# Performance work log

Hardware: AMD Instinct MI355X
Metric: run time of the kernel (lower is better)

## Reference

```python
import jax, jax.numpy as jnp
import numpy as np
import math

HEADS = 32
GROUPS = 8
HEAD_DIM = 64
HIDDEN = 2048
B, S = 2, 2048


def _rope(x, freqs_cis):
    # x: (..., S, head_dim); freqs_cis: (S, head_dim) -> interleaved cos/sin pattern
    x_even = x[..., ::2]
    x_odd = x[..., 1::2]
    cos = freqs_cis[..., ::2]
    sin = freqs_cis[..., 1::2]
    r_even = x_even * cos - x_odd * sin
    r_odd = x_even * sin + x_odd * cos
    return jnp.stack([r_even, r_odd], axis=-1).reshape(x.shape)


def setup_inputs() -> dict:
    key = jax.random.key(0)
    ks = jax.random.split(key, 12)
    scale = 1.0 / math.sqrt(HIDDEN)
    x = jax.random.normal(ks[0], (B, S, HIDDEN), dtype=jnp.float32)
    freqs_cis = jax.random.uniform(ks[1], (S, HEAD_DIM), dtype=jnp.float32)
    causal = jnp.tril(jnp.ones((S, S), dtype=bool))
    mask = jnp.where(causal, 0.0, -1e9).astype(jnp.float32)
    kv_dims = HEAD_DIM * GROUPS
    wq = jax.random.normal(ks[2], (HIDDEN, HIDDEN), jnp.float32) * scale
    bq = jnp.zeros((HIDDEN,), jnp.float32)
    wk = jax.random.normal(ks[3], (kv_dims, HIDDEN), jnp.float32) * scale
    bk = jnp.zeros((kv_dims,), jnp.float32)
    wv = jax.random.normal(ks[4], (kv_dims, HIDDEN), jnp.float32) * scale
    bv = jnp.zeros((kv_dims,), jnp.float32)
    wo = jax.random.normal(ks[5], (HIDDEN, HIDDEN), jnp.float32) * scale
    bo = jnp.zeros((HIDDEN,), jnp.float32)
    return dict(x=x, freqs_cis=freqs_cis, mask=mask, wq=wq, bq=bq,
                wk=wk, bk=bk, wv=wv, bv=bv, wo=wo, bo=bo)


def reference(x, freqs_cis, mask, wq, bq, wk, bk, wv, bv, wo, bo):
    b, s, h = x.shape
    rep = HEADS // GROUPS
    q = x @ wq.T + bq                      # (B,S,H)
    k = x @ wk.T + bk                      # (B,S,G*hd)
    v = x @ wv.T + bv
    q = q.reshape(b, s, HEADS, HEAD_DIM).transpose(0, 2, 1, 3)   # (B,Hh,S,hd)
    k = k.reshape(b, s, GROUPS, HEAD_DIM).transpose(0, 2, 1, 3)  # (B,G,S,hd)
    v = v.reshape(b, s, GROUPS, HEAD_DIM).transpose(0, 2, 1, 3)
    q = _rope(q, freqs_cis)
    k = _rope(k, freqs_cis)
    # GQA: group q heads instead of materially repeating K/V
    qg = q.reshape(b, GROUPS, rep, s, HEAD_DIM)
    scores = jnp.einsum('bgrsd,bgtd->bgrst', qg, k) / math.sqrt(HEAD_DIM)
    scores = scores + mask                 # broadcast (S,S)
    attn = jax.nn.softmax(scores, axis=-1)
    out = jnp.einsum('bgrst,bgtd->bgrsd', attn, v)
    out = out.reshape(b, HEADS, s, HEAD_DIM).transpose(0, 2, 1, 3).reshape(b, s, h)
    return out @ wo.T + bo
```

## Files before the change

### kernel.cpp

```cpp
#include <hip/hip_runtime.h>

#define S_LEN 2048
#define HID   2048
#define NQH   32
#define NKV   8
#define HD    64

typedef __bf16 bf16x8 __attribute__((ext_vector_type(8)));
typedef __bf16 bf16x4 __attribute__((ext_vector_type(4)));
typedef float  f32x4  __attribute__((ext_vector_type(4)));

#define MFMA16(a, b, c) __builtin_amdgcn_mfma_f32_16x16x32_bf16(a, b, c, 0, 0, 0)

__device__ __forceinline__ void async_copy16(const void* g, void* l) {
  __builtin_amdgcn_global_load_lds(
      (const __attribute__((address_space(1))) unsigned int*)g,
      (__attribute__((address_space(3))) unsigned int*)l, 16, 0, 0);
}

__global__ void cast_all_k(const float* __restrict__ x,  const float* __restrict__ wq,
                           const float* __restrict__ wk, const float* __restrict__ wv,
                           const float* __restrict__ wo,
                           __bf16* __restrict__ xb,  __bf16* __restrict__ wqb,
                           __bf16* __restrict__ wkb, __bf16* __restrict__ wvb,
                           __bf16* __restrict__ wob) {
  int bid = blockIdx.x;
  const float* in; __bf16* out; int base;
  if (bid < 8192)       { in = x;  out = xb;  base = bid; }
  else if (bid < 12288) { in = wq; out = wqb; base = bid - 8192; }
  else if (bid < 13312) { in = wk; out = wkb; base = bid - 12288; }
  else if (bid < 14336) { in = wv; out = wvb; base = bid - 13312; }
  else                  { in = wo; out = wob; base = bid - 14336; }
  int i = (base * 256 + threadIdx.x) * 4;
  float4 v = *(const float4*)(in + i);
  bf16x4 o;
  o[0] = (__bf16)v.x; o[1] = (__bf16)v.y; o[2] = (__bf16)v.z; o[3] = (__bf16)v.w;
  *(bf16x4*)(out + i) = o;
}

__device__ __forceinline__ void gemm_core(const __bf16* __restrict__ A, const __bf16* __restrict__ B,
                                          int m0, int n0, int K,
                                          __bf16 (&Asm)[128][32], __bf16 (&Bsm)[128][32],
                                          f32x4 (&acc)[4][4]) {
  const int tid = threadIdx.x, wave = tid >> 6, lane = tid & 63;
  const int l15 = lane & 15, quad = lane >> 4;
  const int wr = wave >> 1, wc = wave & 1;
  const int lrow = lane >> 2, lcol = (lane & 3) * 8;

  const __bf16* ag = A + (size_t)(m0 + wave * 32 + lrow) * K + lcol;
  const __bf16* bg = B + (size_t)(n0 + wave * 32 + lrow) * K + lcol;
  __bf16* al = &Asm[wave * 32][0];
  __bf16* bl = &Bsm[wave * 32][0];
  const size_t rowstep = (size_t)16 * K;

  for (int kt = 0; kt < K; kt += 32) {
    __syncthreads();
    async_copy16(ag + kt, al);
    async_copy16(ag + kt + rowstep, al + 16 * 32);
    async_copy16(bg + kt, bl);
    async_copy16(bg + kt + rowstep, bl + 16 * 32);
    __syncthreads();
    bf16x8 af[4], bfr[4];
#pragma unroll
    for (int mt = 0; mt < 4; mt++)
      af[mt] = *(const bf16x8*)&Asm[wr * 64 + mt * 16 + l15][quad * 8];
#pragma unroll
    for (int nt = 0; nt < 4; nt++)
      bfr[nt] = *(const bf16x8*)&Bsm[wc * 64 + nt * 16 + l15][quad * 8];
#pragma unroll
    for (int mt = 0; mt < 4; mt++)
#pragma unroll
      for (int nt = 0; nt < 4; nt++)
        acc[mt][nt] = MFMA16(af[mt], bfr[nt], acc[mt][nt]);
  }
}

__global__ __launch_bounds__(256) void gemm_qkv_k(const __bf16* __restrict__ xb,
    const __bf16* __restrict__ wqb, const __bf16* __restrict__ wkb, const __bf16* __restrict__ wvb,
    const float* __restrict__ bq, const float* __restrict__ bk, const float* __restrict__ bv,
    const float* __restrict__ fr,
    __bf16* __restrict__ Qb, __bf16* __restrict__ Kb, __bf16* __restrict__ Vt) {
  __shared__ __align__(16) __bf16 Asm[128][32];
  __shared__ __align__(16) __bf16 Bsm[128][32];
  const int by = blockIdx.y;
  const int m0 = blockIdx.x * 128;
  const __bf16* B; const float* bias; int n0;
  int mode;
  if (by < 16)      { B = wqb; bias = bq; n0 = by * 128;        mode = 0; }
  else if (by < 20) { B = wkb; bias = bk; n0 = (by - 16) * 128; mode = 1; }
  else              { B = wvb; bias = bv; n0 = (by - 20) * 128; mode = 2; }

  f32x4 acc[4][4] = {};
  gemm_core(xb, B, m0, n0, HID, Asm, Bsm, acc);

  const int tid = threadIdx.x, wave = tid >> 6, lane = tid & 63;
  const int l15 = lane & 15, quad = lane >> 4;
  const int wr = wave >> 1, wc = wave & 1;

  if (mode == 2) {
#pragma unroll
    for (int nt = 0; nt < 4; nt++) {
      int col = n0 + wc * 64 + nt * 16 + l15;
      int g = col >> 6, d = col & 63;
      float bv2 = bias[col];
#pragma unroll
      for (int mt = 0; mt < 4; mt++) {
        int row = m0 + wr * 64 + mt * 16 + quad * 4;
        int b = row >> 11, s = row & 2047;
        bf16x4 o;
#pragma unroll
        for (int r = 0; r < 4; r++) o[r] = (__bf16)(acc[mt][nt][r] + bv2);
        *(bf16x4*)(Vt + (((size_t)(b * NKV + g) * HD + d)) * S_LEN + s) = o;
      }
    }
  } else {
    const float scale = (mode == 0) ? 0.125f * 1.44269504f : 1.0f;
    const int ldc = (mode == 0) ? HID : 512;
    __bf16* C = (mode == 0) ? Qb : Kb;
    const int dpar = l15 & 1;
#pragma unroll
    for (int nt = 0; nt < 4; nt++) {
      int col = n0 + wc * 64 + nt * 16 + l15;
      int d = col & 63;
      float bv2 = bias[col];
#pragma unroll
      for (int mt = 0; mt < 4; mt++) {
        int row = m0 + wr * 64 + mt * 16 + quad * 4;
        int s = row & 2047;
#pragma unroll
        for (int r = 0; r < 4; r++) {
          float v = acc[mt][nt][r] + bv2;
          float p = __shfl_xor(v, 1, 64);
          float f = fr[(size_t)(s + r) * HD + d];
          float fp = __shfl_xor(f, 1, 64);
          float o = dpar ? (p * f + v * fp) : (v * f - p * fp);
          C[(size_t)(row + r) * ldc + col] = (__bf16)(o * scale);
        }
      }
    }
  }
}

__global__ __launch_bounds__(256) void gemm_out_k(const __bf16* __restrict__ A,
    const __bf16* __restrict__ Bw, const float* __restrict__ bias, float* __restrict__ C) {
  __shared__ __align__(16) __bf16 Asm[128][32];
  __shared__ __align__(16) __bf16 Bsm[128][32];
  const int m0 = blockIdx.x * 128, n0 = blockIdx.y * 128;
  f32x4 acc[4][4] = {};
  gemm_core(A, Bw, m0, n0, HID, Asm, Bsm, acc);
  const int tid = threadIdx.x, wave = tid >> 6, lane = tid & 63;
  const int l15 = lane & 15, quad = lane >> 4;
  const int wr = wave >> 1, wc = wave & 1;
#pragma unroll
  for (int nt = 0; nt < 4; nt++) {
    int col = n0 + wc * 64 + nt * 16 + l15;
    float bv = bias[col];
#pragma unroll
    for (int mt = 0; mt < 4; mt++) {
      int row = m0 + wr * 64 + mt * 16 + quad * 4;
#pragma unroll
      for (int r = 0; r < 4; r++)
        C[(size_t)(row + r) * HID + col] = acc[mt][nt][r] + bv;
    }
  }
}

__global__ __launch_bounds__(256) void flash_k(const __bf16* __restrict__ Q,
                                               const __bf16* __restrict__ K,
                                               const __bf16* __restrict__ Vt,
                                               __bf16* __restrict__ O) {
  __shared__ __align__(16) __bf16 Ksm[64][64];
  __shared__ __align__(16) __bf16 Vsm[64][64];
  __shared__ __align__(16) __bf16 Psm[4][32][64];
  const int tid = threadIdx.x;
  const int wave = tid >> 6, lane = tid & 63;
  const int l15 = lane & 15, quad = lane >> 4;
  const int x7 = l15 & 7;
  const int bh = blockIdx.x;
  const int qt = 15 - blockIdx.y;
  const int b = bh >> 5, h = bh & 31, g = h >> 2;
  const int q0 = qt * 128;
  const int wq0 = q0 + wave * 32;

  bf16x8 qf[2][2];
#pragma unroll
  for (int mt = 0; mt < 2; mt++) {
    const __bf16* qp = Q + ((size_t)(b * S_LEN + wq0 + mt * 16 + l15)) * HID + h * HD + quad * 8;
    qf[mt][0] = *(const bf16x8*)qp;
    qf[mt][1] = *(const bf16x8*)(qp + 32);
  }

  f32x4 acc[2][4] = {};
  float rsum[2][4] = {};

  const int srow = tid >> 2, sc = (tid & 3) * 16;
  const int r7 = srow & 7;
  const int w0 = (((sc >> 3))     ^ r7) * 8;
  const int w1 = (((sc >> 3) + 1) ^ r7) * 8;

  const __bf16* kbase = K + ((size_t)b * S_LEN) * (NKV * HD) + g * HD;
  const __bf16* vrow  = Vt + (((size_t)b * NKV + g) * HD + srow) * S_LEN;

  const int tmax = 2 * qt + 1;
  uint4 k0, k1, v0, v1;
  {
    const __bf16* kp = kbase + (size_t)srow * (NKV * HD) + sc;
    k0 = *(const uint4*)kp; k1 = *(const uint4*)(kp + 8);
    const __bf16* vp = vrow + sc;
    v0 = *(const uint4*)vp; v1 = *(const uint4*)(vp + 8);
  }

  for (int t = 0; t <= tmax; t++) {
    const int kv0 = t * 64;
    __syncthreads();
    *(uint4*)&Ksm[srow][w0] = k0;
    *(uint4*)&Ksm[srow][w1] = k1;
    *(uint4*)&Vsm[srow][w0] = v0;
    *(uint4*)&Vsm[srow][w1] = v1;
    if (t < tmax) {
      const int kv0n = kv0 + 64;
      const __bf16* kp = kbase + (size_t)(kv0n + srow) * (NKV * HD) + sc;
      k0 = *(const uint4*)kp; k1 = *(const uint4*)(kp + 8);
      const __bf16* vp = vrow + kv0n + sc;
      v0 = *(const uint4*)vp; v1 = *(const uint4*)(vp + 8);
    }
    __syncthreads();

    if (kv0 > wq0 + 31) continue;

    bf16x8 kf[2][4];
#pragma unroll
    for (int ks = 0; ks < 2; ks++)
#pragma unroll
      for (int nt = 0; nt < 4; nt++)
        kf[ks][nt] = *(const bf16x8*)&Ksm[nt * 16 + l15][((ks * 4 + quad) ^ x7) * 8];

    const bool domask = (kv0 + 63 > wq0);
#pragma unroll
    for (int mt = 0; mt < 2; mt++) {
      f32x4 sacc[4] = {};
#pragma unroll
      for (int nt = 0; nt < 4; nt++) {
        sacc[nt] = MFMA16(qf[mt][0], kf[0][nt], sacc[nt]);
        sacc[nt] = MFMA16(qf[mt][1], kf[1][nt], sacc[nt]);
      }
#pragma unroll
      for (int nt = 0; nt < 4; nt++) {
        int kv = kv0 + nt * 16 + l15;
        int qr = wq0 + mt * 16 + quad * 4;
#pragma unroll
        for (int r = 0; r < 4; r++) {
          float p = __builtin_exp2f(sacc[nt][r]);
          if (domask && kv > qr + r) p = 0.f;
          rsum[mt][r] += p;
          int prow = mt * 16 + quad * 4 + r;
          Psm[wave][prow][(((nt * 2 + (l15 >> 3)) ^ (prow & 7)) * 8) + (l15 & 7)] = (__bf16)p;
        }
      }
    }

#pragma unroll
    for (int ks = 0; ks < 2; ks++) {
      bf16x8 vf[4];
#pragma unroll
      for (int nt = 0; nt < 4; nt++)
        vf[nt] = *(const bf16x8*)&Vsm[nt * 16 + l15][((ks * 4 + quad) ^ x7) * 8];
#pragma unroll
      for (int mt = 0; mt < 2; mt++) {
        bf16x8 pf = *(const bf16x8*)&Psm[wave][mt * 16 + l15][((ks * 4 + quad) ^ x7) * 8];
#pragma unroll
        for (int nt = 0; nt < 4; nt++)
          acc[mt][nt] = MFMA16(pf, vf[nt], acc[mt][nt]);
      }
    }
  }

#pragma unroll
  for (int mt = 0; mt < 2; mt++)
#pragma unroll
    for (int off = 1; off < 16; off <<= 1)
#pragma unroll
      for (int r = 0; r < 4; r++)
        rsum[mt][r] += __shfl_xor(rsum[mt][r], off, 64);

#pragma unroll
  for (int mt = 0; mt < 2; mt++) {
    __bf16* op = O + ((size_t)(b * S_LEN + wq0 + mt * 16 + quad * 4)) * HID + h * HD;
    float inv[4];
#pragma unroll
    for (int r = 0; r < 4; r++) inv[r] = 1.f / rsum[mt][r];
#pragma unroll
    for (int nt = 0; nt < 4; nt++)
#pragma unroll
      for (int r = 0; r < 4; r++)
        op[(size_t)r * HID + nt * 16 + l15] = (__bf16)(acc[mt][nt][r] * inv[r]);
  }
}

extern "C" void kernel_launch(void* const* d_in, const int* in_sizes, int n_in,
                              void* d_out, int out_size, void* d_ws, size_t ws_size,
                              hipStream_t stream) {
  (void)in_sizes; (void)n_in; (void)out_size; (void)ws_size;
  const float* x  = (const float*)d_in[0];
  const float* fr = (const float*)d_in[1];
  const float* wq = (const float*)d_in[3];
  const float* bq = (const float*)d_in[4];
  const float* wk = (const float*)d_in[5];
  const float* bk = (const float*)d_in[6];
  const float* wv = (const float*)d_in[7];
  const float* bv = (const float*)d_in[8];
  const float* wo = (const float*)d_in[9];
  const float* bo = (const float*)d_in[10];
  float* out = (float*)d_out;
  char* ws = (char*)d_ws;

  __bf16* xb  = (__bf16*)(ws);
  __bf16* wqb = (__bf16*)(ws + ((size_t)16 << 20));
  __bf16* wkb = (__bf16*)(ws + ((size_t)24 << 20));
  __bf16* wvb = (__bf16*)(ws + ((size_t)26 << 20));
  __bf16* wob = (__bf16*)(ws + ((size_t)28 << 20));
  __bf16* Qb  = (__bf16*)(ws + ((size_t)36 << 20));
  __bf16* Kb  = (__bf16*)(ws + ((size_t)52 << 20));
  __bf16* Vtb = (__bf16*)(ws + ((size_t)60 << 20));
  __bf16* Ab  = (__bf16*)(ws + ((size_t)64 << 20));

  cast_all_k<<<18432, 256, 0, stream>>>(x, wq, wk, wv, wo, xb, wqb, wkb, wvb, wob);

  gemm_qkv_k<<<dim3(32, 24), 256, 0, stream>>>(xb, wqb, wkb, wvb, bq, bk, bv, fr, Qb, Kb, Vtb);

  flash_k<<<dim3(64, 16), 256, 0, stream>>>(Qb, Kb, Vtb, Ab);

  gemm_out_k<<<dim3(32, 16), 256, 0, stream>>>(Ab, wob, bo, out);
}
```

Before: 358.8 us.

## Compute softmax row sums with MFMA against ones and precompute LDS byte offsets

The per-element float row-sum accumulation and the final cross-lane shuffle reduction are replaced by an extra MFMA that multiplies the bf16 P tile by a vector of ones. The row sums therefore come from the same rounded P values that feed P@V. LDS addressing for K, V and P moves to precomputed byte offsets, and the global K/V pointers are advanced incrementally, which trims address arithmetic in the inner loop. The cost is one extra MFMA per P fragment, and the normalizer now sums bf16-rounded probabilities, a small numerical change.

```diff
diff --git a/kernel.cpp b/kernel.cpp
--- a/kernel.cpp
+++ b/kernel.cpp
@@ -169,18 +169,17 @@
                                                const __bf16* __restrict__ K,
                                                const __bf16* __restrict__ Vt,
                                                __bf16* __restrict__ O) {
-  __shared__ __align__(16) __bf16 Ksm[64][64];
-  __shared__ __align__(16) __bf16 Vsm[64][64];
-  __shared__ __align__(16) __bf16 Psm[4][32][64];
+  __shared__ __align__(64) __bf16 Ksm[64][64];
+  __shared__ __align__(64) __bf16 Vsm[64][64];
+  __shared__ __align__(64) __bf16 Psm[4][32][64];
   const int tid = threadIdx.x;
   const int wave = tid >> 6, lane = tid & 63;
   const int l15 = lane & 15, quad = lane >> 4;
-  const int x7 = l15 & 7;
+  const int x7 = l15 & 7, l15h = l15 >> 3;
   const int bh = blockIdx.x;
   const int qt = 15 - blockIdx.y;
   const int b = bh >> 5, h = bh & 31, g = h >> 2;
-  const int q0 = qt * 128;
-  const int wq0 = q0 + wave * 32;
+  const int wq0 = qt * 128 + wave * 32;
 
   bf16x8 qf[2][2];
 #pragma unroll
@@ -189,27 +188,37 @@
     qf[mt][0] = *(const bf16x8*)qp;
     qf[mt][1] = *(const bf16x8*)(qp + 32);
   }
+  bf16x8 ones;
+#pragma unroll
+  for (int j = 0; j < 8; j++) ones[j] = (__bf16)1.0f;
 
   f32x4 acc[2][4] = {};
-  float rsum[2][4] = {};
+  f32x4 accs[2] = {};
 
   const int srow = tid >> 2, sc = (tid & 3) * 16;
   const int r7 = srow & 7;
   const int w0 = (((sc >> 3))     ^ r7) * 8;
   const int w1 = (((sc >> 3) + 1) ^ r7) * 8;
 
-  const __bf16* kbase = K + ((size_t)b * S_LEN) * (NKV * HD) + g * HD;
-  const __bf16* vrow  = Vt + (((size_t)b * NKV + g) * HD + srow) * S_LEN;
+  char* kbp = (char*)&Ksm[0][0];
+  char* vbp = (char*)&Vsm[0][0];
+  char* pbp = (char*)&Psm[0][0][0];
+  int kr[2], pr[2], pw[4];
+#pragma unroll
+  for (int ks = 0; ks < 2; ks++) {
+    kr[ks] = l15 * 128 + (((ks * 4 + quad) ^ x7) * 16);
+    pr[ks] = wave * 4096 + kr[ks];
+  }
+#pragma unroll
+  for (int nt = 0; nt < 4; nt++)
+    pw[nt] = wave * 4096 + quad * 512 + x7 * 2 + (((2 * nt + l15h) ^ ((quad & 1) * 4)) * 16);
+
+  const __bf16* kp = K + ((size_t)b * S_LEN + srow) * (NKV * HD) + g * HD + sc;
+  const __bf16* vp = Vt + (((size_t)b * NKV + g) * HD + srow) * S_LEN + sc;
+  uint4 k0 = *(const uint4*)kp, k1 = *(const uint4*)(kp + 8);
+  uint4 v0 = *(const uint4*)vp, v1 = *(const uint4*)(vp + 8);
 
   const int tmax = 2 * qt + 1;
-  uint4 k0, k1, v0, v1;
-  {
-    const __bf16* kp = kbase + (size_t)srow * (NKV * HD) + sc;
-    k0 = *(const uint4*)kp; k1 = *(const uint4*)(kp + 8);
-    const __bf16* vp = vrow + sc;
-    v0 = *(const uint4*)vp; v1 = *(const uint4*)(vp + 8);
-  }
-
   for (int t = 0; t <= tmax; t++) {
     const int kv0 = t * 64;
     __syncthreads();
@@ -218,10 +227,8 @@
     *(uint4*)&Vsm[srow][w0] = v0;
     *(uint4*)&Vsm[srow][w1] = v1;
     if (t < tmax) {
-      const int kv0n = kv0 + 64;
-      const __bf16* kp = kbase + (size_t)(kv0n + srow) * (NKV * HD) + sc;
+      kp += 64 * NKV * HD;  vp += 64;
       k0 = *(const uint4*)kp; k1 = *(const uint4*)(kp + 8);
-      const __bf16* vp = vrow + kv0n + sc;
       v0 = *(const uint4*)vp; v1 = *(const uint4*)(vp + 8);
     }
     __syncthreads();
@@ -233,7 +240,7 @@
     for (int ks = 0; ks < 2; ks++)
 #pragma unroll
       for (int nt = 0; nt < 4; nt++)
-        kf[ks][nt] = *(const bf16x8*)&Ksm[nt * 16 + l15][((ks * 4 + quad) ^ x7) * 8];
+        kf[ks][nt] = *(const bf16x8*)(kbp + (kr[ks] + nt * 2048));
 
     const bool domask = (kv0 + 63 > wq0);
 #pragma unroll
@@ -252,9 +259,7 @@
         for (int r = 0; r < 4; r++) {
           float p = __builtin_exp2f(sacc[nt][r]);
           if (domask && kv > qr + r) p = 0.f;
-          rsum[mt][r] += p;
-          int prow = mt * 16 + quad * 4 + r;
-          Psm[wave][prow][(((nt * 2 + (l15 >> 3)) ^ (prow & 7)) * 8) + (l15 & 7)] = (__bf16)p;
+          *(__bf16*)(pbp + ((pw[nt] ^ (r << 4)) + (mt * 2048 + r * 128))) = (__bf16)p;
         }
       }
     }
@@ -264,31 +269,24 @@
       bf16x8 vf[4];
 #pragma unroll
       for (int nt = 0; nt < 4; nt++)
-        vf[nt] = *(const bf16x8*)&Vsm[nt * 16 + l15][((ks * 4 + quad) ^ x7) * 8];
+        vf[nt] = *(const bf16x8*)(vbp + (kr[ks] + nt * 2048));
 #pragma unroll
       for (int mt = 0; mt < 2; mt++) {
-        bf16x8 pf = *(const bf16x8*)&Psm[wave][mt * 16 + l15][((ks * 4 + quad) ^ x7) * 8];
+        bf16x8 pf = *(const bf16x8*)(pbp + (pr[ks] + mt * 2048));
+        accs[mt] = MFMA16(pf, ones, accs[mt]);
 #pragma unroll
         for (int nt = 0; nt < 4; nt++)
           acc[mt][nt] = MFMA16(pf, vf[nt], acc[mt][nt]);
       }
     }
   }
-
-#pragma unroll
-  for (int mt = 0; mt < 2; mt++)
-#pragma unroll
-    for (int off = 1; off < 16; off <<= 1)
-#pragma unroll
-      for (int r = 0; r < 4; r++)
-        rsum[mt][r] += __shfl_xor(rsum[mt][r], off, 64);
 
 #pragma unroll
   for (int mt = 0; mt < 2; mt++) {
     __bf16* op = O + ((size_t)(b * S_LEN + wq0 + mt * 16 + quad * 4)) * HID + h * HD;
     float inv[4];
 #pragma unroll
-    for (int r = 0; r < 4; r++) inv[r] = 1.f / rsum[mt][r];
+    for (int r = 0; r < 4; r++) inv[r] = 1.f / accs[mt][r];
 #pragma unroll
     for (int nt = 0; nt < 4; nt++)
 #pragma unroll
```

Result: no change. 355.0 us (-1.0%).
